# Optimization experiments

Hardware: AMD Instinct MI355X
Metric: run time of the kernel (lower is better)

## Reference

```python
import jax, jax.numpy as jnp
import numpy as np
from jax import lax

B, T, H, W, C = 2, 32, 64, 64, 64
K, KT = 7, 5


def kernel_to_freq_3d(kernel, T, H, W):
    # kernel: (C, k_t, k_h, k_w) -> (C, T, H, W) complex freq (circularly centered)
    Cc, k_t, k_h, k_w = kernel.shape
    t_idx = (jnp.arange(k_t) - k_t // 2) % T
    h_idx = (jnp.arange(k_h) - k_h // 2) % H
    w_idx = (jnp.arange(k_w) - k_w // 2) % W
    tt, th, tw = jnp.meshgrid(t_idx, h_idx, w_idx, indexing='ij')
    padded = jnp.zeros((Cc, T, H, W), dtype=kernel.dtype).at[:, tt, th, tw].set(kernel)
    return jnp.fft.fftn(padded, axes=(1, 2, 3))


def heinsen_scan_log(log_coeffs, log_values):
    def op(left, right):
        a_l, b_l = left
        a_r, b_r = right
        return (a_l + a_r, jnp.logaddexp(a_r + b_l, b_r))
    _, log_h = lax.associative_scan(op, (log_coeffs, log_values), axis=0)
    return log_h


def setup_inputs() -> dict:
    key = jax.random.key(0)
    ks = jax.random.split(key, 9)
    dense_scale = 1.0 / np.sqrt(C)
    kern_scale = 1.0 / np.sqrt(KT * K * K)
    return {
        'x': jax.random.normal(ks[0], (B, T, H, W, C), jnp.float32),
        'gate_w': jax.random.normal(ks[1], (C, C), jnp.float32) * dense_scale,
        'gate_b': jnp.zeros((C,), jnp.float32),
        'hidden_w': jax.random.normal(ks[2], (C, C), jnp.float32) * dense_scale,
        'hidden_b': jnp.zeros((C,), jnp.float32),
        'gate_kernel': jax.random.normal(ks[3], (C, KT, K, K), jnp.float32) * kern_scale,
        'hidden_kernel': jax.random.normal(ks[4], (C, KT, K, K), jnp.float32) * kern_scale,
        'out_w': jax.random.normal(ks[5], (C, C), jnp.float32) * dense_scale,
        'out_b': jnp.zeros((C,), jnp.float32),
    }


def reference(x, gate_w, gate_b, hidden_w, hidden_b, gate_kernel, hidden_kernel, out_w, out_b):
    Bx, Tx, Hx, Wx, Cx = x.shape
    gate_proj = jnp.einsum('bthwc,cd->bthwd', x, gate_w) + gate_b
    hidden_proj = jnp.einsum('bthwc,cd->bthwd', x, hidden_w) + hidden_b
    # kernels to frequency domain, channel-last: (T, H, W, C)
    gk_f = kernel_to_freq_3d(gate_kernel, Tx, Hx, Wx).transpose(1, 2, 3, 0)
    hk_f = kernel_to_freq_3d(hidden_kernel, Tx, Hx, Wx).transpose(1, 2, 3, 0)
    gate_f = jnp.fft.fftn(gate_proj, axes=(1, 2, 3))
    hidden_f = jnp.fft.fftn(hidden_proj, axes=(1, 2, 3))
    gate_spatial = jnp.fft.ifftn(gate_f * gk_f[None], axes=(1, 2, 3)).real
    hidden_spatial = jnp.fft.ifftn(hidden_f * hk_f[None], axes=(1, 2, 3)).real
    # minGRU in log space: h_t = (1-z_t) h_{t-1} + z_t * h~_t
    log_forget = -jax.nn.softplus(gate_spatial)       # log(1 - z)
    log_update = -jax.nn.softplus(-gate_spatial)      # log(z)
    log_hidden = jnp.log(hidden_spatial ** 2 + 1e-06)
    log_values = log_update + log_hidden
    # scan over T (move T to axis 0)
    log_h_seq = heinsen_scan_log(
        log_forget.transpose(1, 0, 2, 3, 4), log_values.transpose(1, 0, 2, 3, 4))
    h = jnp.exp(log_h_seq.transpose(1, 0, 2, 3, 4))
    out = jnp.einsum('bthwc,cd->bthwd', h, out_w) + out_b
    return out.astype(jnp.float32)
```

## Files before the change

kernel.cpp:

```cpp
#include <hip/hip_runtime.h>
#include <hip/hip_fp16.h>

#define NELEM 16777216

typedef _Float16 f16x8 __attribute__((ext_vector_type(8)));
typedef _Float16 h2v  __attribute__((ext_vector_type(2)));
typedef float f32x4 __attribute__((ext_vector_type(4)));

static __device__ __forceinline__ void pk_fma(uint& d, uint a, uint b) {
    asm("v_pk_fma_f16 %0, %1, %2, %0" : "+v"(d) : "v"(a), "v"(b));
}

__global__ __launch_bounds__(256) void proj2_kernel(
    const float* __restrict__ x,
    const float* __restrict__ wg, const float* __restrict__ bg,
    const float* __restrict__ wh, const float* __restrict__ bh,
    uint* __restrict__ pg, uint* __restrict__ ph)
{
    __shared__ __align__(16) _Float16 sX[128 * 64];
    __shared__ __align__(16) _Float16 sWT[2][64 * 64];
    const int tid = threadIdx.x;
    const int row0 = (int)blockIdx.x * 128;

    #pragma unroll
    for (int kci = 0; kci < 4; ++kci) {
        const int chunk = tid + kci * 256;
        const int r = chunk >> 3, q = chunk & 7;
        const float* gp = x + (long long)(row0 + r) * 64 + q * 8;
        const float4 v0 = *reinterpret_cast<const float4*>(gp);
        const float4 v1 = *reinterpret_cast<const float4*>(gp + 4);
        f16x8 hv;
        hv[0] = (_Float16)v0.x; hv[1] = (_Float16)v0.y; hv[2] = (_Float16)v0.z; hv[3] = (_Float16)v0.w;
        hv[4] = (_Float16)v1.x; hv[5] = (_Float16)v1.y; hv[6] = (_Float16)v1.z; hv[7] = (_Float16)v1.w;
        *reinterpret_cast<f16x8*>(&sX[r * 64 + ((q ^ (r & 7)) * 8)]) = hv;
    }
    {
        const int d = tid & 63;
        const int cb = (tid >> 6) * 16;
        #pragma unroll
        for (int i = 0; i < 16; ++i) {
            const int c = cb + i;
            const int off = d * 64 + (((c >> 3) ^ (d & 7)) * 8) + (c & 7);
            sWT[0][off] = (_Float16)wg[c * 64 + d];
            sWT[1][off] = (_Float16)wh[c * 64 + d];
        }
    }
    __syncthreads();

    const int wv = tid >> 6, lm = tid & 15, lg = (tid & 63) >> 4;
    f16x8 bf[2][4][2];
    #pragma unroll
    for (int nt = 0; nt < 4; ++nt) {
        const int d = nt * 16 + lm;
        #pragma unroll
        for (int s = 0; s < 2; ++s) {
            const int off = d * 64 + (((s * 4 + lg) ^ (d & 7)) * 8);
            bf[0][nt][s] = *reinterpret_cast<const f16x8*>(&sWT[0][off]);
            bf[1][nt][s] = *reinterpret_cast<const f16x8*>(&sWT[1][off]);
        }
    }
    f32x4 acc[2][2][4];
    #pragma unroll
    for (int m = 0; m < 2; ++m)
        #pragma unroll
        for (int mt = 0; mt < 2; ++mt)
            #pragma unroll
            for (int nt = 0; nt < 4; ++nt)
                acc[m][mt][nt] = (f32x4){0.f, 0.f, 0.f, 0.f};

    #pragma unroll
    for (int mt = 0; mt < 2; ++mt) {
        const int r = wv * 32 + mt * 16 + lm;
        const f16x8 a0 = *reinterpret_cast<const f16x8*>(&sX[r * 64 + ((lg ^ (r & 7)) * 8)]);
        const f16x8 a1 = *reinterpret_cast<const f16x8*>(&sX[r * 64 + (((4 + lg) ^ (r & 7)) * 8)]);
        #pragma unroll
        for (int nt = 0; nt < 4; ++nt) {
            acc[0][mt][nt] = __builtin_amdgcn_mfma_f32_16x16x32_f16(a0, bf[0][nt][0], acc[0][mt][nt], 0, 0, 0);
            acc[0][mt][nt] = __builtin_amdgcn_mfma_f32_16x16x32_f16(a1, bf[0][nt][1], acc[0][mt][nt], 0, 0, 0);
            acc[1][mt][nt] = __builtin_amdgcn_mfma_f32_16x16x32_f16(a0, bf[1][nt][0], acc[1][mt][nt], 0, 0, 0);
            acc[1][mt][nt] = __builtin_amdgcn_mfma_f32_16x16x32_f16(a1, bf[1][nt][1], acc[1][mt][nt], 0, 0, 0);
        }
    }
    #pragma unroll
    for (int nt = 0; nt < 4; ++nt) {
        const int col = nt * 16 + lm;
        const int pr  = col >> 1;
        const float bgv = bg[col], bhv = bh[col];
        #pragma unroll
        for (int mt = 0; mt < 2; ++mt) {
            const int rb = row0 + wv * 32 + mt * 16 + lg * 4;
            uint pk0[4], pk1[4];
            #pragma unroll
            for (int i = 0; i < 4; ++i) {
                const float v0 = acc[0][mt][nt][i] + bgv;
                const float p0 = __shfl_xor(v0, 1);
                const float v1 = acc[1][mt][nt][i] + bhv;
                const float p1 = __shfl_xor(v1, 1);
                h2v a, c;
                a[0] = (_Float16)((lm & 1) ? p0 : v0); a[1] = (_Float16)((lm & 1) ? v0 : p0);
                c[0] = (_Float16)((lm & 1) ? p1 : v1); c[1] = (_Float16)((lm & 1) ? v1 : p1);
                pk0[i] = __builtin_bit_cast(uint, a);
                pk1[i] = __builtin_bit_cast(uint, c);
            }
            if (!(lm & 1)) {
                *reinterpret_cast<uint4*>(pg + pr * 262144 + rb) = make_uint4(pk0[0], pk0[1], pk0[2], pk0[3]);
                *reinterpret_cast<uint4*>(ph + pr * 262144 + rb) = make_uint4(pk1[0], pk1[1], pk1[2], pk1[3]);
            }
        }
    }
}

__global__ __launch_bounds__(256) void tapconv_kernel(
    const float* __restrict__ gk, const float* __restrict__ hk, uint* __restrict__ taps)
{
    const int i = blockIdx.x * 256 + threadIdx.x;
    if (i >= 17920) return;
    const int kw = i & 7;
    int r = i >> 3;
    const int kth = r % 35;  r /= 35;
    const int p = r & 31;
    const int mat = r >> 5;
    if (kw >= 7) { taps[i] = 0u; return; }
    const float* K = mat ? hk : gk;
    const int tap = kth * 7 + kw;
    h2v hv;
    hv[0] = (_Float16)K[(2 * p) * 245 + tap];
    hv[1] = (_Float16)K[(2 * p + 1) * 245 + tap];
    taps[i] = __builtin_bit_cast(uint, hv);
}

__global__ __launch_bounds__(256, 5) void conv3d_dual_kernel(
    const uint* __restrict__ inG, uint* __restrict__ outG,
    const uint* __restrict__ inH, uint* __restrict__ outH,
    const uint* __restrict__ taps)
{
    __shared__ __align__(16) uint sAll[4 * 1800];

    const int bid = (int)blockIdx.x;
    const int l = ((bid & 7) << 9) | (bid >> 3);
    const int tile = l & 3;
    const int pgrp = (l >> 2) & 7;
    const int t    = (l >> 5) & 31;
    const int b    = (l >> 10) & 1;
    const int mat  = (l >> 11) & 1;
    const int wave = threadIdx.x >> 6;
    const int lane = threadIdx.x & 63;
    const int h0 = (tile >> 1) * 32, w0 = (tile & 1) * 32;
    const int pair = pgrp * 4 + wave;

    const uint* in = mat ? inH : inG;
    uint* out      = mat ? outH : outG;

    uint* tileL = sAll + wave * 1800;
    uint* tapL  = tileL + 1520;

    const uint* gt = taps + (mat * 32 + pair) * 280;
    for (int i = lane; i < 280; i += 64) tapL[i] = gt[i];

    const int iy = lane >> 3, ix = lane & 7;

    uint tot[4][4];
    #pragma unroll
    for (int o = 0; o < 4; ++o)
        #pragma unroll
        for (int j = 0; j < 4; ++j) tot[o][j] = 0u;

    #pragma unroll 1
    for (int kt = 0; kt < 5; ++kt) {
        const int tin = (t - kt + 2) & 31;
        const uint2* pin = reinterpret_cast<const uint2*>(in) +
                           (pair * 131072 + (b * 32 + tin) * 2048);
        #pragma unroll
        for (int ro = 0; ro < 12; ++ro) {
            const int idx = ro * 64 + lane;
            if (idx < 760) {
                const int r  = (idx * 205) >> 12;
                const int c2 = idx - r * 20;
                const int gh = (h0 - 3 + r) & 63;
                const int uc = ((w0 >> 1) - 2 + c2) & 31;
                const uint2 v = pin[gh * 32 + uc];
                *reinterpret_cast<uint2*>(&tileL[r * 40 + c2 * 2]) = v;
            }
        }

        const uint* tkt = tapL + kt * 56;
        uint kv[4][8];

        #pragma unroll
        for (int rr = 0; rr < 10; ++rr) {
            if (rr <= 6) {
                const int kh = 6 - rr;
                const uint4 k0 = *reinterpret_cast<const uint4*>(tkt + kh * 8);
                const uint4 k1 = *reinterpret_cast<const uint4*>(tkt + kh * 8 + 4);
                kv[kh & 3][0] = k0.x; kv[kh & 3][1] = k0.y;
                kv[kh & 3][2] = k0.z; kv[kh & 3][3] = k0.w;
                kv[kh & 3][4] = k1.x; kv[kh & 3][5] = k1.y;
                kv[kh & 3][6] = k1.z; kv[kh & 3][7] = k1.w;
            }
            const uint* rp = &tileL[(4 * iy + rr) * 40 + 4 * ix];
            const uint4 r0 = *reinterpret_cast<const uint4*>(rp);
            const uint4 r1 = *reinterpret_cast<const uint4*>(rp + 4);
            const uint4 r2 = *reinterpret_cast<const uint4*>(rp + 8);
            uint row[12];
            row[0] = r0.x; row[1] = r0.y; row[2]  = r0.z; row[3]  = r0.w;
            row[4] = r1.x; row[5] = r1.y; row[6]  = r1.z; row[7]  = r1.w;
            row[8] = r2.x; row[9] = r2.y; row[10] = r2.z; row[11] = r2.w;

            #pragma unroll
            for (int o = 0; o < 4; ++o) {
                const int kh = o + 6 - rr;
                if (kh < 0 || kh > 6) continue;
                #pragma unroll
                for (int kw = 0; kw < 7; ++kw)
                    #pragma unroll
                    for (int j = 0; j < 4; ++j)
                        pk_fma(tot[o][j], kv[kh & 3][kw], row[j + 7 - kw]);
            }
        }
    }

    uint* ob = out + pair * 262144 + (b * 32 + t) * 4096;
    #pragma unroll
    for (int o = 0; o < 4; ++o)
        *reinterpret_cast<uint4*>(ob + (h0 + 4 * iy + o) * 64 + (w0 + 4 * ix)) =
            make_uint4(tot[o][0], tot[o][1], tot[o][2], tot[o][3]);
}

__global__ __launch_bounds__(256) void scan_kernel(
    const uint* __restrict__ gs, const uint* __restrict__ hs, uint* __restrict__ hout)
{
    const int tid = blockIdx.x * 256 + threadIdx.x;
    const int base = (tid >> 12) * 131072 + (tid & 4095);
    float h0 = 0.f, h1 = 0.f;
    for (int t = 0; t < 32; ++t) {
        const int a = base + t * 4096;
        const float2 g  = __half22float2(__builtin_bit_cast(__half2, gs[a]));
        const float2 hv = __half22float2(__builtin_bit_cast(__half2, hs[a]));
        const float z0 = 1.f / (1.f + __expf(-g.x));
        const float z1 = 1.f / (1.f + __expf(-g.y));
        h0 = fmaf(1.f - z0, h0, z0 * fmaf(hv.x, hv.x, 1e-6f));
        h1 = fmaf(1.f - z1, h1, z1 * fmaf(hv.y, hv.y, 1e-6f));
        hout[a] = __builtin_bit_cast(uint, __floats2half2_rn(h0, h1));
    }
}

__global__ __launch_bounds__(256) void outgemm_kernel(
    const uint* __restrict__ hin, const float* __restrict__ w,
    const float* __restrict__ bias, float* __restrict__ out)
{
    __shared__ __align__(16) uint sXu[128 * 36];
    __shared__ __align__(16) _Float16 sWT[64 * 64];
    const int tid = threadIdx.x;
    const int row0 = (int)blockIdx.x * 128;

    {
        const int pr = tid >> 3, k = tid & 7;
        const uint* src = hin + pr * 262144 + row0 + k * 16;
        #pragma unroll
        for (int q = 0; q < 4; ++q) {
            const uint4 v = *reinterpret_cast<const uint4*>(src + q * 4);
            sXu[(k * 16 + q * 4 + 0) * 36 + pr] = v.x;
            sXu[(k * 16 + q * 4 + 1) * 36 + pr] = v.y;
            sXu[(k * 16 + q * 4 + 2) * 36 + pr] = v.z;
            sXu[(k * 16 + q * 4 + 3) * 36 + pr] = v.w;
        }
    }
    {
        const int d = tid & 63;
        const int cb = (tid >> 6) * 16;
        #pragma unroll
        for (int i = 0; i < 16; ++i) {
            const int c = cb + i;
            sWT[d * 64 + (((c >> 3) ^ (d & 7)) * 8) + (c & 7)] = (_Float16)w[c * 64 + d];
        }
    }
    __syncthreads();

    const int wv = tid >> 6, lm = tid & 15, lg = (tid & 63) >> 4;
    f16x8 bf[4][2];
    #pragma unroll
    for (int nt = 0; nt < 4; ++nt) {
        const int d = nt * 16 + lm;
        #pragma unroll
        for (int s = 0; s < 2; ++s)
            bf[nt][s] = *reinterpret_cast<const f16x8*>(&sWT[d * 64 + (((s * 4 + lg) ^ (d & 7)) * 8)]);
    }
    f32x4 acc[2][4];
    #pragma unroll
    for (int mt = 0; mt < 2; ++mt)
        #pragma unroll
        for (int nt = 0; nt < 4; ++nt)
            acc[mt][nt] = (f32x4){0.f, 0.f, 0.f, 0.f};

    #pragma unroll
    for (int mt = 0; mt < 2; ++mt) {
        const int r = wv * 32 + mt * 16 + lm;
        const f16x8 a0 = *reinterpret_cast<const f16x8*>(&sXu[r * 36 + lg * 4]);
        const f16x8 a1 = *reinterpret_cast<const f16x8*>(&sXu[r * 36 + 16 + lg * 4]);
        #pragma unroll
        for (int nt = 0; nt < 4; ++nt) {
            acc[mt][nt] = __builtin_amdgcn_mfma_f32_16x16x32_f16(a0, bf[nt][0], acc[mt][nt], 0, 0, 0);
            acc[mt][nt] = __builtin_amdgcn_mfma_f32_16x16x32_f16(a1, bf[nt][1], acc[mt][nt], 0, 0, 0);
        }
    }
    #pragma unroll
    for (int nt = 0; nt < 4; ++nt) {
        const int col = nt * 16 + lm;
        const float bv = bias[col];
        #pragma unroll
        for (int mt = 0; mt < 2; ++mt) {
            const long long rb = row0 + wv * 32 + mt * 16 + lg * 4;
            #pragma unroll
            for (int i = 0; i < 4; ++i)
                out[(rb + i) * 64 + col] = acc[mt][nt][i] + bv;
        }
    }
}

extern "C" void kernel_launch(void* const* d_in, const int* in_sizes, int n_in,
                              void* d_out, int out_size, void* d_ws, size_t ws_size,
                              hipStream_t stream)
{
    const float* x  = (const float*)d_in[0];
    const float* gw = (const float*)d_in[1];
    const float* gb = (const float*)d_in[2];
    const float* hw = (const float*)d_in[3];
    const float* hb = (const float*)d_in[4];
    const float* gk = (const float*)d_in[5];
    const float* hk = (const float*)d_in[6];
    const float* ow = (const float*)d_in[7];
    const float* ob = (const float*)d_in[8];

    uint* W1 = (uint*)d_ws;
    uint* W2 = W1 + NELEM / 2;
    uint* W3 = W2 + NELEM / 2;
    uint* taps = W3 + NELEM / 2;
    uint* Dsc = (uint*)d_out;

    tapconv_kernel<<<70, 256, 0, stream>>>(gk, hk, taps);
    proj2_kernel<<<2048, 256, 0, stream>>>(x, gw, gb, hw, hb, W1, W2);
    conv3d_dual_kernel<<<4096, 256, 0, stream>>>(W1, W3, W2, Dsc, taps);
    scan_kernel<<<1024, 256, 0, stream>>>(W3, Dsc, W1);
    outgemm_kernel<<<2048, 256, 0, stream>>>(W1, ow, ob, (float*)d_out);
}
```

Before: 226.8 us.

## Drop LDS staging in conv3d; load rows from global, taps as scalar operands

```diff
diff --git a/kernel.cpp b/kernel.cpp
--- a/kernel.cpp
+++ b/kernel.cpp
@@ -7,8 +7,8 @@
 typedef _Float16 h2v  __attribute__((ext_vector_type(2)));
 typedef float f32x4 __attribute__((ext_vector_type(4)));
 
-static __device__ __forceinline__ void pk_fma(uint& d, uint a, uint b) {
-    asm("v_pk_fma_f16 %0, %1, %2, %0" : "+v"(d) : "v"(a), "v"(b));
+static __device__ __forceinline__ void pk_fma_sv(uint& d, uint a_s, uint b_v) {
+    asm("v_pk_fma_f16 %0, %1, %2, %0" : "+v"(d) : "s"(a_s), "v"(b_v));
 }
 
 __global__ __launch_bounds__(256) void proj2_kernel(
@@ -129,13 +129,11 @@
     taps[i] = __builtin_bit_cast(uint, hv);
 }
 
-__global__ __launch_bounds__(256, 5) void conv3d_dual_kernel(
+__global__ __launch_bounds__(256) void conv3d_dual_kernel(
     const uint* __restrict__ inG, uint* __restrict__ outG,
     const uint* __restrict__ inH, uint* __restrict__ outH,
     const uint* __restrict__ taps)
 {
-    __shared__ __align__(16) uint sAll[4 * 1800];
-
     const int bid = (int)blockIdx.x;
     const int l = ((bid & 7) << 9) | (bid >> 3);
     const int tile = l & 3;
@@ -151,13 +149,15 @@
     const uint* in = mat ? inH : inG;
     uint* out      = mat ? outH : outG;
 
-    uint* tileL = sAll + wave * 1800;
-    uint* tapL  = tileL + 1520;
-
-    const uint* gt = taps + (mat * 32 + pair) * 280;
-    for (int i = lane; i < 280; i += 64) tapL[i] = gt[i];
-
     const int iy = lane >> 3, ix = lane & 7;
+
+    const int tapOff = __builtin_amdgcn_readfirstlane((mat * 32 + pair) * 280);
+    const uint* tb = taps + tapOff;
+    const int pbOff = __builtin_amdgcn_readfirstlane(pair * 262144 + b * 131072);
+
+    int colu[3];
+    #pragma unroll
+    for (int m = 0; m < 3; ++m) colu[m] = (w0 + 4 * ix - 4 + 4 * m) & 63;
 
     uint tot[4][4];
     #pragma unroll
@@ -168,44 +168,31 @@
     #pragma unroll 1
     for (int kt = 0; kt < 5; ++kt) {
         const int tin = (t - kt + 2) & 31;
-        const uint2* pin = reinterpret_cast<const uint2*>(in) +
-                           (pair * 131072 + (b * 32 + tin) * 2048);
-        #pragma unroll
-        for (int ro = 0; ro < 12; ++ro) {
-            const int idx = ro * 64 + lane;
-            if (idx < 760) {
-                const int r  = (idx * 205) >> 12;
-                const int c2 = idx - r * 20;
-                const int gh = (h0 - 3 + r) & 63;
-                const int uc = ((w0 >> 1) - 2 + c2) & 31;
-                const uint2 v = pin[gh * 32 + uc];
-                *reinterpret_cast<uint2*>(&tileL[r * 40 + c2 * 2]) = v;
-            }
-        }
-
-        const uint* tkt = tapL + kt * 56;
-        uint kv[4][8];
+        const uint* pin = in + pbOff + tin * 4096;
+        const uint* tkt = tb + kt * 56;
+
+        uint kv[7][8];
+        #pragma unroll
+        for (int kh = 6; kh >= 5; --kh)
+            #pragma unroll
+            for (int i2 = 0; i2 < 8; ++i2) kv[kh][i2] = tkt[kh * 8 + i2];
 
         #pragma unroll
         for (int rr = 0; rr < 10; ++rr) {
-            if (rr <= 6) {
-                const int kh = 6 - rr;
-                const uint4 k0 = *reinterpret_cast<const uint4*>(tkt + kh * 8);
-                const uint4 k1 = *reinterpret_cast<const uint4*>(tkt + kh * 8 + 4);
-                kv[kh & 3][0] = k0.x; kv[kh & 3][1] = k0.y;
-                kv[kh & 3][2] = k0.z; kv[kh & 3][3] = k0.w;
-                kv[kh & 3][4] = k1.x; kv[kh & 3][5] = k1.y;
-                kv[kh & 3][6] = k1.z; kv[kh & 3][7] = k1.w;
-            }
-            const uint* rp = &tileL[(4 * iy + rr) * 40 + 4 * ix];
-            const uint4 r0 = *reinterpret_cast<const uint4*>(rp);
-            const uint4 r1 = *reinterpret_cast<const uint4*>(rp + 4);
-            const uint4 r2 = *reinterpret_cast<const uint4*>(rp + 8);
+            if (rr <= 4) {
+                const int kh = 4 - rr;
+                #pragma unroll
+                for (int i2 = 0; i2 < 8; ++i2) kv[kh][i2] = tkt[kh * 8 + i2];
+            }
+            const int gh = (h0 - 3 + 4 * iy + rr) & 63;
+            const int rowu = gh * 64;
             uint row[12];
-            row[0] = r0.x; row[1] = r0.y; row[2]  = r0.z; row[3]  = r0.w;
-            row[4] = r1.x; row[5] = r1.y; row[6]  = r1.z; row[7]  = r1.w;
-            row[8] = r2.x; row[9] = r2.y; row[10] = r2.z; row[11] = r2.w;
-
+            #pragma unroll
+            for (int m = 0; m < 3; ++m) {
+                const uint4 v = *reinterpret_cast<const uint4*>(pin + rowu + colu[m]);
+                row[4 * m]     = v.x; row[4 * m + 1] = v.y;
+                row[4 * m + 2] = v.z; row[4 * m + 3] = v.w;
+            }
             #pragma unroll
             for (int o = 0; o < 4; ++o) {
                 const int kh = o + 6 - rr;
@@ -214,7 +201,7 @@
                 for (int kw = 0; kw < 7; ++kw)
                     #pragma unroll
                     for (int j = 0; j < 4; ++j)
-                        pk_fma(tot[o][j], kv[kh & 3][kw], row[j + 7 - kw]);
+                        pk_fma_sv(tot[o][j], kv[kh][kw], row[j + 7 - kw]);
             }
         }
     }
```

Result: faster. 207.6 us, median of 2 (-8.5%).
